# Optimization experiments

Measured on AMD Instinct MI355X. Metric: run time of the kernel, lower is better.

Reference implementation:

```python
import jax, jax.numpy as jnp
import numpy as np

B, C, D, H, W = 4, 1, 128, 192, 192


def setup_inputs() -> dict:
    key = jax.random.key(0)
    ks = jax.random.split(key, 8)
    x = jax.random.normal(ks[0], (B, C, D, H, W), jnp.float32)
    y = jax.random.normal(ks[1], (B, C, H, W), jnp.float32)
    rot_0 = jax.random.normal(ks[2], (B, 1), jnp.float32) * 0.1
    rot_1 = jax.random.normal(ks[3], (B, 1), jnp.float32) * 0.1
    rot_2 = jax.random.normal(ks[4], (B, 1), jnp.float32) * 0.1
    trans_1 = jax.random.normal(ks[5], (B, 1), jnp.float32) * 0.05
    trans_2 = jax.random.normal(ks[6], (B, 1), jnp.float32) * 0.05
    center_point = (jnp.tile(jnp.array([[D / 2., H / 2., W / 2.]], jnp.float32), (B, 1))
                    + jax.random.normal(ks[7], (B, 3), jnp.float32))
    return {"x": x, "y": y, "rot_0": rot_0, "rot_1": rot_1, "rot_2": rot_2,
            "trans_1": trans_1, "trans_2": trans_2, "center_point": center_point}


def _euler2mat(a):
    # a: [B,3] angles (z, y, x), ZYX intrinsic composition as in source
    z, y, x = a[:, 0], a[:, 1], a[:, 2]
    cz, sz = jnp.cos(z), jnp.sin(z)
    cy, sy = jnp.cos(y), jnp.sin(y)
    cx, sx = jnp.cos(x), jnp.sin(x)
    o = jnp.ones_like(z)
    zr = jnp.zeros_like(z)
    zmat = jnp.stack([cz, -sz, zr, sz, cz, zr, zr, zr, o], 1).reshape(-1, 3, 3)
    ymat = jnp.stack([cy, zr, sy, zr, o, zr, -sy, zr, cy], 1).reshape(-1, 3, 3)
    xmat = jnp.stack([o, zr, zr, zr, cx, -sx, zr, sx, cx], 1).reshape(-1, 3, 3)
    return zmat @ ymat @ xmat


def _rigid4x4(rot3, t):
    # rot3: [B,3,3], t: [B,3] -> [B,4,4]
    bn = rot3.shape[0]
    top = jnp.concatenate([rot3, t[:, :, None]], axis=-1)          # [B,3,4]
    bot = jnp.broadcast_to(jnp.array([[[0., 0., 0., 1.]]], jnp.float32), (bn, 1, 4))
    return jnp.concatenate([top, bot], axis=1)


def _trans_mat(t):
    bn = t.shape[0]
    eye = jnp.broadcast_to(jnp.eye(3, dtype=jnp.float32), (bn, 3, 3))
    return _rigid4x4(eye, t)


def _affine_grid(mat, shape):
    # mat: [B,4,4]; voxel-coordinate grid (nitorch convention): g = R @ c + t
    d, h, w = shape
    zz, yy, xx = jnp.meshgrid(jnp.arange(d, dtype=jnp.float32),
                              jnp.arange(h, dtype=jnp.float32),
                              jnp.arange(w, dtype=jnp.float32), indexing='ij')
    coords = jnp.stack([zz, yy, xx], axis=-1)                      # [D,H,W,3]
    return (jnp.einsum('dhwj,bij->bdhwi', coords, mat[:, :3, :3])
            + mat[:, None, None, None, :3, 3])                    # [B,D,H,W,3]


def _grid_pull_one(vol, g):
    # vol: [C,D,H,W]; g: [D,H,W,3] voxel coords; trilinear, zero boundary
    d, h, w = vol.shape[1], vol.shape[2], vol.shape[3]
    g0f = jnp.floor(g)
    frac = g - g0f
    g0 = g0f.astype(jnp.int32)
    out = jnp.zeros((vol.shape[0],) + g.shape[:-1], vol.dtype)
    for dz in (0, 1):
        wz = frac[..., 0] if dz else 1. - frac[..., 0]
        iz = g0[..., 0] + dz
        for dy in (0, 1):
            wy = frac[..., 1] if dy else 1. - frac[..., 1]
            iy = g0[..., 1] + dy
            for dx in (0, 1):
                wx = frac[..., 2] if dx else 1. - frac[..., 2]
                ix = g0[..., 2] + dx
                valid = ((iz >= 0) & (iz < d) & (iy >= 0) & (iy < h)
                         & (ix >= 0) & (ix < w)).astype(vol.dtype)
                v = vol[:, jnp.clip(iz, 0, d - 1), jnp.clip(iy, 0, h - 1),
                        jnp.clip(ix, 0, w - 1)]                   # [C,D,H,W]
                out = out + v * (wz * wy * wx * valid)[None]
    return out


def reference(x, y, rot_0, rot_1, rot_2, trans_1, trans_2, center_point):
    d, h, w = x.shape[2], x.shape[3], x.shape[4]
    t1 = _trans_mat(-center_point)
    t2 = _trans_mat(center_point)
    # first translation component is detached*0 -> exact zeros
    trans = jnp.concatenate([jnp.zeros_like(trans_1), trans_1 * h, trans_2 * w], axis=1)
    angles = jnp.concatenate([rot_0, rot_1, rot_2], axis=1)
    rot = _euler2mat(angles)
    rigid = _rigid4x4(rot, trans)
    mat = t2 @ (rigid @ t1)                                        # center-about-point rigid
    grid = _affine_grid(mat, (d, h, w))                            # [B,D,H,W,3]
    x_warp = jax.vmap(_grid_pull_one)(x, grid)                     # [B,C,D,H,W]
    x_2d = jnp.mean(x_warp, axis=2)                                # [B,C,H,W]
    return (x_2d, x_warp, y)
```

## Files before the change

kernel.cpp:

```cpp
#include <hip/hip_runtime.h>

#define Bn 4
#define Dd 128
#define Hh 192
#define Ww 192

#define PLANE (Hh * Ww)
#define VOL   (Dd * PLANE)
#define N2D   (Bn * PLANE)
#define WARP_OFF ((size_t)N2D)
#define Y_OFF (WARP_OFF + (size_t)Bn * VOL)

#define DT 16
#define HT 8
#define WT 32
#define NDB (Dd / DT)
#define NHB (Hh / HT)
#define NWB (Ww / WT)
#define NBLK (Bn * NDB * NHB * NWB)
#define NCH (NDB * 2)

#define SZ 25
#define SY 16
#define SXP 48
#define ZSTRIDE (SY * SXP)
#define LDSF (SZ * ZSTRIDE)

typedef float f2 __attribute__((ext_vector_type(2)));
typedef f2 __attribute__((aligned(4))) f2u;
__device__ __forceinline__ f2 load2(const float* p) { return *(const f2u*)p; }

__device__ __forceinline__ void gload_lds16(const float* g, float* l) {
    __builtin_amdgcn_global_load_lds(
        (const __attribute__((address_space(1))) void*)g,
        (__attribute__((address_space(3))) void*)l,
        16, 0, 0);
}

__global__ __launch_bounds__(256) void tbl_kernel(const float* __restrict__ rot0,
                                                  const float* __restrict__ rot1,
                                                  const float* __restrict__ rot2,
                                                  const float* __restrict__ tr1,
                                                  const float* __restrict__ tr2,
                                                  const float* __restrict__ cp,
                                                  float* __restrict__ tbl) {
    const int id = blockIdx.x * 256 + threadIdx.x;
    if (id >= NBLK) return;
    const int wblk = id % NWB;
    const int t1   = id / NWB;
    const int hblk = t1 % NHB;
    const int t2   = t1 / NHB;
    const int dblk = t2 & (NDB - 1);
    const int b    = t2 >> 3;

    const float z = rot0[b], y = rot1[b], x = rot2[b];
    const float cz = cosf(z), sz = sinf(z);
    const float cy = cosf(y), sy = sinf(y);
    const float cx = cosf(x), sx = sinf(x);
    const float A0 = cz * cy;
    const float B0 = -sz * cx + cz * sy * sx;
    const float C0 = sz * sx + cz * sy * cx;
    const float A1 = sz * cy;
    const float B1 = cz * cx + sz * sy * sx;
    const float C1 = -cz * sx + sz * sy * cx;
    const float A2 = -sy;
    const float B2 = cy * sx;
    const float C2 = cy * cx;
    const float c0 = cp[b * 3 + 0], c1 = cp[b * 3 + 1], c2 = cp[b * 3 + 2];
    const float E0 = -(A0 * c0 + B0 * c1 + C0 * c2) + c0;
    const float E1 = -(A1 * c0 + B1 * c1 + C1 * c2) + tr1[b] * (float)Hh + c1;
    const float E2 = -(A2 * c0 + B2 * c1 + C2 * c2) + tr2[b] * (float)Ww + c2;

    const int d0 = dblk * DT, h0 = hblk * HT, w0 = wblk * WT;
    const float dlo = (float)d0, dhi = (float)(d0 + DT - 1);
    const float hlo = (float)h0, hhi = (float)(h0 + HT - 1);
    const float wlo = (float)w0, whi = (float)(w0 + WT - 1);

    const float loZ = E0 + fminf(A0 * dlo, A0 * dhi) + fminf(B0 * hlo, B0 * hhi) + fminf(C0 * wlo, C0 * whi);
    const float hiZ = E0 + fmaxf(A0 * dlo, A0 * dhi) + fmaxf(B0 * hlo, B0 * hhi) + fmaxf(C0 * wlo, C0 * whi);
    const float loY = E1 + fminf(A1 * dlo, A1 * dhi) + fminf(B1 * hlo, B1 * hhi) + fminf(C1 * wlo, C1 * whi);
    const float hiY = E1 + fmaxf(A1 * dlo, A1 * dhi) + fmaxf(B1 * hlo, B1 * hhi) + fmaxf(C1 * wlo, C1 * whi);
    const float loX = E2 + fminf(A2 * dlo, A2 * dhi) + fminf(B2 * hlo, B2 * hhi) + fminf(C2 * wlo, C2 * whi);
    const float hiX = E2 + fmaxf(A2 * dlo, A2 * dhi) + fmaxf(B2 * hlo, B2 * hhi) + fmaxf(C2 * wlo, C2 * whi);

    const int lz = (int)floorf(loZ) - 1;
    const int hz = (int)floorf(hiZ) + 2;
    const int ly = (int)floorf(loY) - 1;
    const int hy = (int)floorf(hiY) + 2;
    const int lx4 = ((int)floorf(loX) - 1) & ~3;
    const int hx = (int)floorf(hiX) + 2;

    const int hzrel = hz - lz;
    const bool fits = (hzrel <= SZ - 1) && (hy - ly <= SY - 1) && (hx - lx4 <= SXP - 2);
    const bool interior = (loZ >= 0.01f) && (hiZ < (float)(Dd - 1) - 0.01f) &&
                          (loY >= 0.01f) && (hiY < (float)(Hh - 1) - 0.01f) &&
                          (loX >= 0.01f) && (hiX < (float)(Ww - 1) - 0.01f);

    const float bz = E0 + A0 * dlo + B0 * hlo + C0 * wlo - (float)lz;
    const float by = E1 + A1 * dlo + B1 * hlo + C1 * wlo - (float)ly;
    const float bx = E2 + A2 * dlo + B2 * hlo + C2 * wlo - (float)lx4;

    float* T = tbl + (size_t)id * 16;
    T[0] = A0; T[1] = B0; T[2]  = C0; T[3]  = bz;
    T[4] = A1; T[5] = B1; T[6]  = C1; T[7]  = by;
    T[8] = A2; T[9] = B2; T[10] = C2; T[11] = bx;
    int* TI = (int*)T;
    TI[12] = lz; TI[13] = ly; TI[14] = lx4;
    TI[15] = (fits ? 1 : 0) | (interior ? 2 : 0) |
             (b << 2) | (dblk << 4) | (hblk << 7) | (wblk << 12) | (min(hzrel, 127) << 15);
}

template <bool WP>
__global__ __launch_bounds__(512) void warp_tiled(const float* __restrict__ x,
                                                  const float* __restrict__ tbl,
                                                  float* __restrict__ out,
                                                  float* __restrict__ partial) {
    __shared__ __align__(16) float box[LDSF];

    const int g  = blockIdx.x;
    const int wl = (g & 7) * (NBLK / 8) + (g >> 3);

    const float4* T4 = (const float4*)(tbl + (size_t)wl * 16);
    const float4 r0 = T4[0], r1 = T4[1], r2 = T4[2];
    const int4   r3 = ((const int4*)T4)[3];
    const int lz = r3.x, ly = r3.y, lx4 = r3.z, fl = r3.w;
    const bool fits = fl & 1, interior = fl & 2;
    const int b     = (fl >> 2) & 3;
    const int dblk  = (fl >> 4) & 7;
    const int hblk  = (fl >> 7) & 31;
    const int wblk  = (fl >> 12) & 7;
    const int hzrel = (fl >> 15) & 127;
    const int d0 = dblk * DT, h0 = hblk * HT, w0 = wblk * WT;

    const float A0 = r0.x, B0 = r0.y, C0 = r0.z, bz = r0.w;
    const float A1 = r1.x, B1 = r1.y, C1 = r1.z, by = r1.w;
    const float A2 = r2.x, B2 = r2.y, C2 = r2.z, bx = r2.w;

    const int t = threadIdx.x;
    const int w_in = t & 31;
    const int h_in = (t >> 5) & 7;
    const int dq   = t >> 8;
    const int lane = t & 63;
    const int wid  = t >> 6;

    const float fh = (float)h_in, fw = (float)w_in, fdq = (float)(dq * 8);
    const float fz0 = bz + B0 * fh + C0 * fw + A0 * fdq;
    const float fy0 = by + B1 * fh + C1 * fw + A1 * fdq;
    const float fx0 = bx + B2 * fh + C2 * fw + A2 * fdq;

    const float* __restrict__ V = x + (size_t)b * VOL;
    float* __restrict__ obase = out + WARP_OFF + (size_t)b * VOL +
                                (size_t)(d0 + dq * 8) * PLANE +
                                (size_t)(h0 + h_in) * Ww + (w0 + w_in);

    float sum = 0.0f;

    if (fits) {
        const int r0i = lane / 12,             c0i = (lane - r0i * 12) * 4;
        const int i1  = 64 + lane;  const int r1i = i1 / 12, c1i = (i1 - r1i * 12) * 4;
        const int i2  = 128 + lane; const int r2i = i2 / 12, c2i = (i2 - r2i * 12) * 4;
        const int yy0 = ly + r0i, xx0 = lx4 + c0i;
        const int yy1 = ly + r1i, xx1 = lx4 + c1i;
        const int yy2 = ly + r2i, xx2 = lx4 + c2i;
        const bool ok0 = ((unsigned)yy0 < (unsigned)Hh) && ((unsigned)xx0 <= (unsigned)(Ww - 4));
        const bool ok1 = ((unsigned)yy1 < (unsigned)Hh) && ((unsigned)xx1 <= (unsigned)(Ww - 4));
        const bool ok2 = ((unsigned)yy2 < (unsigned)Hh) && ((unsigned)xx2 <= (unsigned)(Ww - 4));
        const int off0 = yy0 * Ww + xx0;
        const int off1 = yy1 * Ww + xx1;
        const int off2 = yy2 * Ww + xx2;

        if (!interior) {
            const float4 z4 = {0.0f, 0.0f, 0.0f, 0.0f};
            for (int i = 4 * t; i < LDSF; i += 4 * 512) *(float4*)&box[i] = z4;
            __syncthreads();
        }

        for (int zrel = wid; zrel <= hzrel; zrel += 8) {
            const int zz = lz + zrel;
            if ((unsigned)zz < (unsigned)Dd) {
                const float* Vz = V + (size_t)zz * PLANE;
                float* Lz = box + zrel * ZSTRIDE;
                if (ok0) gload_lds16(Vz + off0, Lz);
                if (ok1) gload_lds16(Vz + off1, Lz + 256);
                if (ok2) gload_lds16(Vz + off2, Lz + 512);
            }
        }

        int   basev[8];
        float txv[8], tyv[8], tzv[8];
        #pragma unroll
        for (int j = 0; j < 8; ++j) {
            const float fd = (float)j;
            const float gz = fmaf(A0, fd, fz0);
            const float gy = fmaf(A1, fd, fy0);
            const float gx = fmaf(A2, fd, fx0);
            const float fz = floorf(gz), fy = floorf(gy), fx = floorf(gx);
            tzv[j] = gz - fz; tyv[j] = gy - fy; txv[j] = gx - fx;
            basev[j] = (int)fz * ZSTRIDE + (int)fy * SXP + (int)fx;
        }
        __syncthreads();

        #pragma unroll
        for (int j = 0; j < 8; ++j) {
            const int base = basev[j];
            const f2 qa = load2(&box[base]);
            const f2 qb = load2(&box[base + SXP]);
            const f2 qc = load2(&box[base + ZSTRIDE]);
            const f2 qd = load2(&box[base + ZSTRIDE + SXP]);

            const float tx = txv[j], ty = tyv[j], tz = tzv[j];
            const float wx0 = 1.0f - tx, wy0 = 1.0f - ty, wz0 = 1.0f - tz;
            const float v00 = fmaf(wx0, qa.x, tx * qa.y);
            const float v01 = fmaf(wx0, qb.x, tx * qb.y);
            const float v10 = fmaf(wx0, qc.x, tx * qc.y);
            const float v11 = fmaf(wx0, qd.x, tx * qd.y);
            const float vz0 = fmaf(wy0, v00, ty * v01);
            const float vz1 = fmaf(wy0, v10, ty * v11);
            const float val = fmaf(wz0, vz0, tz * vz1);

            __builtin_nontemporal_store(val, obase + (size_t)j * PLANE);
            sum += val;
        }
    } else {
        const float fz0a = fz0 + (float)lz;
        const float fy0a = fy0 + (float)ly;
        const float fx0a = fx0 + (float)lx4;
        #pragma unroll 4
        for (int j = 0; j < 8; ++j) {
            const float fd = (float)j;
            const float gz = fmaf(A0, fd, fz0a);
            const float gy = fmaf(A1, fd, fy0a);
            const float gx = fmaf(A2, fd, fx0a);

            const float fz = floorf(gz), fy = floorf(gy), fx = floorf(gx);
            const float tz = gz - fz, ty = gy - fy, tx = gx - fx;
            const int iz = (int)fz, iy = (int)fy, ix = (int)fx;

            const float wz0 = ((unsigned)iz       < (unsigned)Dd) ? (1.0f - tz) : 0.0f;
            const float wz1 = ((unsigned)(iz + 1) < (unsigned)Dd) ? tz : 0.0f;
            const float wy0 = ((unsigned)iy       < (unsigned)Hh) ? (1.0f - ty) : 0.0f;
            const float wy1 = ((unsigned)(iy + 1) < (unsigned)Hh) ? ty : 0.0f;
            const float wx0 = ((unsigned)ix       < (unsigned)Ww) ? (1.0f - tx) : 0.0f;
            const float wx1 = ((unsigned)(ix + 1) < (unsigned)Ww) ? tx : 0.0f;

            const bool right  = (ix >= Ww - 1);
            const bool leftok = (ix >= 0);
            const float WL = (right ? 0.0f : wx0) + (leftok ? 0.0f : wx1);
            const float WH = (right ? wx0 : 0.0f) + (leftok ? wx1 : 0.0f);

            const int iz0c = min(max(iz, 0), Dd - 1);
            const int iz1c = min(max(iz + 1, 0), Dd - 1);
            const int iy0c = min(max(iy, 0), Hh - 1);
            const int iy1c = min(max(iy + 1, 0), Hh - 1);
            const int ixl  = min(max(ix, 0), Ww - 2);

            const f2 q00 = load2(V + (size_t)iz0c * PLANE + iy0c * Ww + ixl);
            const f2 q01 = load2(V + (size_t)iz0c * PLANE + iy1c * Ww + ixl);
            const f2 q10 = load2(V + (size_t)iz1c * PLANE + iy0c * Ww + ixl);
            const f2 q11 = load2(V + (size_t)iz1c * PLANE + iy1c * Ww + ixl);

            const float v00 = fmaf(WL, q00.x, WH * q00.y);
            const float v01 = fmaf(WL, q01.x, WH * q01.y);
            const float v10 = fmaf(WL, q10.x, WH * q10.y);
            const float v11 = fmaf(WL, q11.x, WH * q11.y);

            const float vz0 = fmaf(wy0, v00, wy1 * v01);
            const float vz1 = fmaf(wy0, v10, wy1 * v11);
            const float val = fmaf(wz0, vz0, wz1 * vz1);

            __builtin_nontemporal_store(val, obase + (size_t)j * PLANE);
            sum += val;
        }
    }

    if (WP) {
        const int ch = dblk * 2 + dq;
        partial[((size_t)(b * NCH + ch) * Hh + (h0 + h_in)) * Ww + (w0 + w_in)] = sum;
    }
}

__global__ __launch_bounds__(256) void reduce_kernel(const float* __restrict__ partial,
                                                     const float* __restrict__ yin,
                                                     float* __restrict__ out) {
    const int q = blockIdx.x * 256 + threadIdx.x;
    if (q >= N2D / 4) return;
    const int idx = q * 4;
    const int b = idx / PLANE;
    const int rem = idx - b * PLANE;
    const float* p = partial + (size_t)b * NCH * PLANE + rem;
    float4 s = {0.0f, 0.0f, 0.0f, 0.0f};
    #pragma unroll
    for (int c = 0; c < NCH; ++c) {
        const float4 v = *(const float4*)(p + (size_t)c * PLANE);
        s.x += v.x; s.y += v.y; s.z += v.z; s.w += v.w;
    }
    const float inv = 1.0f / (float)Dd;
    s.x *= inv; s.y *= inv; s.z *= inv; s.w *= inv;
    *(float4*)(out + idx) = s;
    *(float4*)(out + Y_OFF + idx) = *(const float4*)(yin + idx);
}

__global__ __launch_bounds__(256) void reduce_fallback_kernel(const float* __restrict__ yin,
                                                              float* __restrict__ out) {
    const int idx = blockIdx.x * 256 + threadIdx.x;
    if (idx >= N2D) return;
    const int b = idx / PLANE;
    const int rem = idx - b * PLANE;
    const float* p = out + WARP_OFF + (size_t)b * VOL + rem;
    float s = 0.0f;
    #pragma unroll 8
    for (int d = 0; d < Dd; ++d) s += p[(size_t)d * PLANE];
    out[idx] = s * (1.0f / (float)Dd);
    out[Y_OFF + idx] = yin[idx];
}

extern "C" void kernel_launch(void* const* d_in, const int* in_sizes, int n_in,
                              void* d_out, int out_size, void* d_ws, size_t ws_size,
                              hipStream_t stream) {
    const float* x    = (const float*)d_in[0];
    const float* yin  = (const float*)d_in[1];
    const float* rot0 = (const float*)d_in[2];
    const float* rot1 = (const float*)d_in[3];
    const float* rot2 = (const float*)d_in[4];
    const float* tr1  = (const float*)d_in[5];
    const float* tr2  = (const float*)d_in[6];
    const float* cp   = (const float*)d_in[7];

    float* tbl = (float*)d_ws;
    float* partial = tbl + (size_t)NBLK * 16;
    const size_t need = ((size_t)NBLK * 16 + (size_t)Bn * NCH * PLANE) * sizeof(float);

    tbl_kernel<<<(NBLK + 255) / 256, 256, 0, stream>>>(rot0, rot1, rot2, tr1, tr2, cp, tbl);

    if (ws_size >= need) {
        warp_tiled<true><<<NBLK, 512, 0, stream>>>(x, tbl, (float*)d_out, partial);
        reduce_kernel<<<(N2D / 4 + 255) / 256, 256, 0, stream>>>(partial, yin, (float*)d_out);
    } else {
        warp_tiled<false><<<NBLK, 512, 0, stream>>>(x, tbl, (float*)d_out, partial);
        reduce_fallback_kernel<<<(N2D + 255) / 256, 256, 0, stream>>>(yin, (float*)d_out);
    }
}
```

Before: 50.72 us.

## Replace per-chunk partial-sum buffer with fixed-point integer atomic accumulation

```diff
diff --git a/kernel.cpp b/kernel.cpp
--- a/kernel.cpp
+++ b/kernel.cpp
@@ -18,7 +18,9 @@
 #define NHB (Hh / HT)
 #define NWB (Ww / WT)
 #define NBLK (Bn * NDB * NHB * NWB)
-#define NCH (NDB * 2)
+
+#define FPSCALE 1048576.0f
+#define INV_FPD (1.0f / (FPSCALE * (float)Dd))
 
 #define SZ 25
 #define SY 16
@@ -43,8 +45,19 @@
                                                   const float* __restrict__ tr1,
                                                   const float* __restrict__ tr2,
                                                   const float* __restrict__ cp,
-                                                  float* __restrict__ tbl) {
+                                                  float* __restrict__ tbl,
+                                                  int* __restrict__ acc) {
     const int id = blockIdx.x * 256 + threadIdx.x;
+
+    {
+        const int4 z4 = {0, 0, 0, 0};
+        int base = id * 32;
+        if (base < N2D) {
+            #pragma unroll
+            for (int i = 0; i < 8; ++i) *(int4*)(acc + base + 4 * i) = z4;
+        }
+    }
+
     if (id >= NBLK) return;
     const int wblk = id % NWB;
     const int t1   = id / NWB;
@@ -110,11 +123,10 @@
              (b << 2) | (dblk << 4) | (hblk << 7) | (wblk << 12) | (min(hzrel, 127) << 15);
 }
 
-template <bool WP>
 __global__ __launch_bounds__(512) void warp_tiled(const float* __restrict__ x,
                                                   const float* __restrict__ tbl,
                                                   float* __restrict__ out,
-                                                  float* __restrict__ partial) {
+                                                  int* __restrict__ acc) {
     __shared__ __align__(16) float box[LDSF];
 
     const int g  = blockIdx.x;
@@ -273,45 +285,24 @@
         }
     }
 
-    if (WP) {
-        const int ch = dblk * 2 + dq;
-        partial[((size_t)(b * NCH + ch) * Hh + (h0 + h_in)) * Ww + (w0 + w_in)] = sum;
-    }
-}
-
-__global__ __launch_bounds__(256) void reduce_kernel(const float* __restrict__ partial,
+    const int pix = (b * Hh + (h0 + h_in)) * Ww + (w0 + w_in);
+    atomicAdd(acc + pix, (int)rintf(sum * FPSCALE));
+}
+
+__global__ __launch_bounds__(256) void reduce_kernel(const int* __restrict__ acc,
                                                      const float* __restrict__ yin,
                                                      float* __restrict__ out) {
     const int q = blockIdx.x * 256 + threadIdx.x;
     if (q >= N2D / 4) return;
     const int idx = q * 4;
-    const int b = idx / PLANE;
-    const int rem = idx - b * PLANE;
-    const float* p = partial + (size_t)b * NCH * PLANE + rem;
-    float4 s = {0.0f, 0.0f, 0.0f, 0.0f};
-    #pragma unroll
-    for (int c = 0; c < NCH; ++c) {
-        const float4 v = *(const float4*)(p + (size_t)c * PLANE);
-        s.x += v.x; s.y += v.y; s.z += v.z; s.w += v.w;
-    }
-    const float inv = 1.0f / (float)Dd;
-    s.x *= inv; s.y *= inv; s.z *= inv; s.w *= inv;
+    const int4 a = *(const int4*)(acc + idx);
+    float4 s;
+    s.x = (float)a.x * INV_FPD;
+    s.y = (float)a.y * INV_FPD;
+    s.z = (float)a.z * INV_FPD;
+    s.w = (float)a.w * INV_FPD;
     *(float4*)(out + idx) = s;
     *(float4*)(out + Y_OFF + idx) = *(const float4*)(yin + idx);
-}
-
-__global__ __launch_bounds__(256) void reduce_fallback_kernel(const float* __restrict__ yin,
-                                                              float* __restrict__ out) {
-    const int idx = blockIdx.x * 256 + threadIdx.x;
-    if (idx >= N2D) return;
-    const int b = idx / PLANE;
-    const int rem = idx - b * PLANE;
-    const float* p = out + WARP_OFF + (size_t)b * VOL + rem;
-    float s = 0.0f;
-    #pragma unroll 8
-    for (int d = 0; d < Dd; ++d) s += p[(size_t)d * PLANE];
-    out[idx] = s * (1.0f / (float)Dd);
-    out[Y_OFF + idx] = yin[idx];
 }
 
 extern "C" void kernel_launch(void* const* d_in, const int* in_sizes, int n_in,
@@ -327,16 +318,11 @@
     const float* cp   = (const float*)d_in[7];
 
     float* tbl = (float*)d_ws;
-    float* partial = tbl + (size_t)NBLK * 16;
-    const size_t need = ((size_t)NBLK * 16 + (size_t)Bn * NCH * PLANE) * sizeof(float);
-
-    tbl_kernel<<<(NBLK + 255) / 256, 256, 0, stream>>>(rot0, rot1, rot2, tr1, tr2, cp, tbl);
-
-    if (ws_size >= need) {
-        warp_tiled<true><<<NBLK, 512, 0, stream>>>(x, tbl, (float*)d_out, partial);
-        reduce_kernel<<<(N2D / 4 + 255) / 256, 256, 0, stream>>>(partial, yin, (float*)d_out);
-    } else {
-        warp_tiled<false><<<NBLK, 512, 0, stream>>>(x, tbl, (float*)d_out, partial);
-        reduce_fallback_kernel<<<(N2D + 255) / 256, 256, 0, stream>>>(yin, (float*)d_out);
-    }
-}
+    int*   acc = (int*)(tbl + (size_t)NBLK * 16);
+    const size_t need = ((size_t)NBLK * 16 + (size_t)N2D) * sizeof(float);
+    (void)need; (void)ws_size;
+
+    tbl_kernel<<<(NBLK + 255) / 256, 256, 0, stream>>>(rot0, rot1, rot2, tr1, tr2, cp, tbl, acc);
+    warp_tiled<<<NBLK, 512, 0, stream>>>(x, tbl, (float*)d_out, acc);
+    reduce_kernel<<<(N2D / 4 + 255) / 256, 256, 0, stream>>>(acc, yin, (float*)d_out);
+}
```

Result: faster. 49.43 us (-2.5%).
